# Optimization experiments

Hardware: AMD Instinct MI355X
Metric: run time of the kernel (lower is better)

## Reference

```python
import jax, jax.numpy as jnp
import numpy as np

D, H, W = 96, 320, 320          # sparse voxel grid spatial shape
N = 150000                      # number of active voxels
C_IN, C_OUT = 64, 64
EPS = 1e-5
NEG_SLOPE = 0.01


def setup_inputs() -> dict:
    key = jax.random.key(0)
    k1, k2 = jax.random.split(key)
    # unique active voxel coordinates (no collisions), like a real sparse tensor
    rng = np.random.default_rng(0)
    lin = rng.choice(D * H * W, size=N, replace=False)
    z, rem = lin // (H * W), lin % (H * W)
    y, x = rem // W, rem % W
    coords = jnp.asarray(np.stack([z, y, x], axis=1), dtype=jnp.int32)  # [N,3]
    features = jax.random.normal(k1, (N, C_IN), dtype=jnp.float32)
    # conv weight: one [Cin,Cout] matrix per 3x3x3 kernel offset
    weight = jax.random.normal(k2, (27, C_IN, C_OUT), dtype=jnp.float32) * (1.0 / np.sqrt(27 * C_IN))
    gamma = jnp.ones((C_OUT,), dtype=jnp.float32)
    beta = jnp.zeros((C_OUT,), dtype=jnp.float32)
    return {"features": features, "coords": coords, "weight": weight, "gamma": gamma, "beta": beta}


def reference(features, coords, weight, gamma, beta):
    # Submanifold sparse 3D conv: output sites == input sites (active voxels).
    # Build dense index grid: voxel coord -> row index in `features`, -1 if inactive.
    grid = jnp.full((D, H, W), -1, dtype=jnp.int32)
    grid = grid.at[coords[:, 0], coords[:, 1], coords[:, 2]].set(
        jnp.arange(features.shape[0], dtype=jnp.int32))

    out = jnp.zeros((features.shape[0], weight.shape[2]), dtype=features.dtype)
    k = 0
    for dz in (-1, 0, 1):
        for dy in (-1, 0, 1):
            for dx in (-1, 0, 1):
                nz = coords[:, 0] + dz
                ny = coords[:, 1] + dy
                nx = coords[:, 2] + dx
                inb = ((nz >= 0) & (nz < D) & (ny >= 0) & (ny < H)
                       & (nx >= 0) & (nx < W))
                idx = grid[jnp.clip(nz, 0, D - 1),
                           jnp.clip(ny, 0, H - 1),
                           jnp.clip(nx, 0, W - 1)]          # [N]
                valid = inb & (idx >= 0)
                gathered = jnp.where(valid[:, None],
                                     features[jnp.maximum(idx, 0)], 0.0)  # [N,Cin]
                out = out + gathered @ weight[k]             # gather-GEMM-scatter
                k += 1

    # BatchNorm1d (training-mode batch stats, biased variance) + LeakyReLU(0.01)
    mean = jnp.mean(out, axis=0)
    var = jnp.mean(jnp.square(out - mean), axis=0)
    xhat = (out - mean) * jax.lax.rsqrt(var + EPS)
    y = xhat * gamma + beta
    return jnp.where(y >= 0, y, NEG_SLOPE * y)
```

## Files before the change

kernel.cpp:

```cpp
#include <hip/hip_runtime.h>


#define DD 96
#define HH 320
#define WW 320
#define GRID_ELEMS (DD * HH * WW)
#define OCC_WORDS (GRID_ELEMS / 32)
#define CIN 64
#define COUT 64
#define PAIR_CAP 16384
#define STAGE_CAP 40
#define TILE_R 128
#define FSTRIDE 68
#define EPSV 1e-5f
#define SLOPE 0.01f

__global__ void scatter_k(const int* __restrict__ coords, int* __restrict__ grid,
                          unsigned* __restrict__ occ, int N) {
    int i = blockIdx.x * 256 + threadIdx.x;
    if (i >= N) return;
    int z = coords[3 * i], y = coords[3 * i + 1], x = coords[3 * i + 2];
    int l = (z * HH + y) * WW + x;
    grid[l] = i;
    atomicOr(&occ[l >> 5], 1u << (l & 31));
}

__global__ void rulebook_k(const int* __restrict__ coords, const int* __restrict__ grid,
                           const unsigned* __restrict__ occ,
                           int* __restrict__ cnt, int2* __restrict__ pairs, int N) {
    __shared__ int scnt[27];
    __shared__ int sbase[27];
    __shared__ int2 stage[27][STAGE_CAP];
    int tid = threadIdx.x;
    if (tid < 27) scnt[tid] = 0;
    __syncthreads();

    int i = blockIdx.x * 256 + tid;
    if (i < N) {
        int z = coords[3 * i], y = coords[3 * i + 1], x = coords[3 * i + 2];
        int lo = x > 0 ? x - 1 : 0;
        int hi = x < WW - 1 ? x + 1 : WW - 1;
        int wlo = lo >> 5, whi = hi >> 5;

        unsigned wa[9], wb9[9];
        int rwb[9];
#pragma unroll
        for (int r = 0; r < 9; ++r) {
            int zz = z + r / 3 - 1;
            int yy = y + r % 3 - 1;
            bool ok = ((unsigned)zz < DD) && ((unsigned)yy < HH);
            int base = (zz * HH + yy) * WW;
            rwb[r] = base;
            int wbase = base >> 5;
            wa[r]  = ok ? occ[wbase + wlo] : 0u;
            wb9[r] = ok ? occ[wbase + whi] : 0u;
        }
#pragma unroll
        for (int r = 0; r < 9; ++r) {
            for (int xx = lo; xx <= hi; ++xx) {
                if (r == 4 && xx == x) continue;
                unsigned w = ((xx >> 5) == wlo) ? wa[r] : wb9[r];
                if ((w >> (xx & 31)) & 1u) {
                    int j = grid[rwb[r] + xx];
                    int k = r * 3 + (xx - x + 1);
                    int pos = atomicAdd(&scnt[k], 1);
                    if (pos < STAGE_CAP) stage[k][pos] = make_int2(i, j);
                }
            }
        }
    }
    __syncthreads();
    if (tid < 27) {
        int c = scnt[tid];
        if (c > STAGE_CAP) c = STAGE_CAP;
        scnt[tid] = c;
        if (c > 0) sbase[tid] = atomicAdd(&cnt[tid * 32], c);
    }
    __syncthreads();
    for (int s = tid; s < 27 * STAGE_CAP; s += 256) {
        int k = s / STAGE_CAP, p = s % STAGE_CAP;
        if (p < scnt[k]) {
            int pos = sbase[k] + p;
            if (pos < PAIR_CAP) pairs[k * PAIR_CAP + pos] = stage[k][p];
        }
    }
}

__global__ void __launch_bounds__(256) center_k(const float* __restrict__ feat,
                                                const float* __restrict__ w13,
                                                float* __restrict__ out, int N) {
    __shared__ float wl[CIN * COUT];
    __shared__ float fl[TILE_R * FSTRIDE];
    {
        const float4* ws4 = (const float4*)w13;
        float4* wl4 = (float4*)wl;
        for (int t = threadIdx.x; t < CIN * COUT / 4; t += 256) wl4[t] = ws4[t];
    }
    int base_row = blockIdx.x * TILE_R;
    for (int t = threadIdx.x; t < TILE_R * 16; t += 256) {
        int r = t >> 4, c4 = t & 15;
        int gr = base_row + r;
        float4 v = (gr < N) ? ((const float4*)feat)[(size_t)gr * 16 + c4]
                            : make_float4(0.f, 0.f, 0.f, 0.f);
        *(float4*)&fl[r * FSTRIDE + c4 * 4] = v;
    }
    __syncthreads();

    int g = threadIdx.x >> 3;
    int c0 = (threadIdx.x & 7) * 8;
    float4 acc[4][2];
#pragma unroll
    for (int r = 0; r < 4; ++r) {
        acc[r][0] = make_float4(0.f, 0.f, 0.f, 0.f);
        acc[r][1] = make_float4(0.f, 0.f, 0.f, 0.f);
    }
#pragma unroll 4
    for (int ci4 = 0; ci4 < 16; ++ci4) {
        float4 f[4];
#pragma unroll
        for (int r = 0; r < 4; ++r)
            f[r] = *(const float4*)&fl[(g + 32 * r) * FSTRIDE + ci4 * 4];
#pragma unroll
        for (int u = 0; u < 4; ++u) {
            float4 wa = *(const float4*)&wl[(ci4 * 4 + u) * COUT + c0];
            float4 wb = *(const float4*)&wl[(ci4 * 4 + u) * COUT + c0 + 4];
#pragma unroll
            for (int r = 0; r < 4; ++r) {
                float fv = (&f[r].x)[u];
                acc[r][0].x += fv * wa.x;
                acc[r][0].y += fv * wa.y;
                acc[r][0].z += fv * wa.z;
                acc[r][0].w += fv * wa.w;
                acc[r][1].x += fv * wb.x;
                acc[r][1].y += fv * wb.y;
                acc[r][1].z += fv * wb.z;
                acc[r][1].w += fv * wb.w;
            }
        }
    }
    float4* o4 = (float4*)out;
#pragma unroll
    for (int r = 0; r < 4; ++r) {
        int row = base_row + g + 32 * r;
        if (row < N) {
            size_t base = (size_t)row * 16 + (c0 >> 2);
            o4[base] = acc[r][0];
            o4[base + 1] = acc[r][1];
        }
    }
}

__global__ void __launch_bounds__(256) offset_k(const float* __restrict__ feat,
                                                const float* __restrict__ weight,
                                                const int2* __restrict__ pairs,
                                                const int* __restrict__ cnt,
                                                float* __restrict__ out) {
    int k = blockIdx.y;
    if (k >= 13) ++k;
    int ck = cnt[k * 32];
    if (ck > PAIR_CAP) ck = PAIR_CAP;
    if ((int)blockIdx.x * 8 >= ck) return;
    __shared__ float wl[CIN * COUT];
    {
        const float4* ws4 = (const float4*)(weight + (size_t)k * CIN * COUT);
        float4* wl4 = (float4*)wl;
        for (int t = threadIdx.x; t < CIN * COUT / 4; t += 256) wl4[t] = ws4[t];
    }
    __syncthreads();
    int wave = threadIdx.x >> 6;
    int lane = threadIdx.x & 63;
    for (int p0 = (int)blockIdx.x * 8 + wave * 2; p0 < ck; p0 += (int)gridDim.x * 8) {
        bool hasB = (p0 + 1) < ck;
        int2 prA = pairs[k * PAIR_CAP + p0];
        int2 prB = pairs[k * PAIR_CAP + (hasB ? p0 + 1 : p0)];
        const float4* frA = (const float4*)(feat + (size_t)prA.y * CIN);
        const float4* frB = (const float4*)(feat + (size_t)prB.y * CIN);
        float accA = 0.f, accB = 0.f;
#pragma unroll
        for (int ci4 = 0; ci4 < 16; ++ci4) {
            float4 fa = frA[ci4];
            float4 fb = frB[ci4];
#pragma unroll
            for (int u = 0; u < 4; ++u) {
                float w = wl[(ci4 * 4 + u) * COUT + lane];
                accA += (&fa.x)[u] * w;
                accB += (&fb.x)[u] * w;
            }
        }
        atomicAdd(&out[(size_t)prA.x * COUT + lane], accA);
        if (hasB) atomicAdd(&out[(size_t)prB.x * COUT + lane], accB);
    }
}

__global__ void stats_k(const float* __restrict__ out, float* __restrict__ stats, int N) {
    __shared__ float ssum[4][64];
    __shared__ float ssq[4][64];
    int c = threadIdx.x & 63, g = threadIdx.x >> 6;
    float s = 0.f, q = 0.f;
    for (int r = blockIdx.x * 4 + g; r < N; r += gridDim.x * 4) {
        float v = out[(size_t)r * 64 + c];
        s += v;
        q += v * v;
    }
    ssum[g][c] = s;
    ssq[g][c] = q;
    __syncthreads();
    if (threadIdx.x < 64) {
        float ts = ssum[0][c] + ssum[1][c] + ssum[2][c] + ssum[3][c];
        float tq = ssq[0][c] + ssq[1][c] + ssq[2][c] + ssq[3][c];
        atomicAdd(&stats[c * 32], ts);
        atomicAdd(&stats[(64 + c) * 32], tq);
    }
}

__global__ void norm_k(float* __restrict__ out, const float* __restrict__ stats,
                       const float* __restrict__ gamma, const float* __restrict__ beta, int N) {
    int idx = (int)blockIdx.x * 256 + threadIdx.x;
    int total = N * (COUT / 4);
    if (idx >= total) return;
    int c0 = (idx & 15) * 4;
    float inv = 1.0f / (float)N;
    float4 v = ((const float4*)out)[idx];
    float4 r;
#pragma unroll
    for (int u = 0; u < 4; ++u) {
        int c = c0 + u;
        float mean = stats[c * 32] * inv;
        float var = stats[(64 + c) * 32] * inv - mean * mean;
        if (var < 0.f) var = 0.f;
        float sc = gamma[c] * rsqrtf(var + EPSV);
        float sh = beta[c] - mean * sc;
        float y = (&v.x)[u] * sc + sh;
        (&r.x)[u] = (y >= 0.f) ? y : SLOPE * y;
    }
    ((float4*)out)[idx] = r;
}

extern "C" void kernel_launch(void* const* d_in, const int* in_sizes, int n_in,
                              void* d_out, int out_size, void* d_ws, size_t ws_size,
                              hipStream_t stream) {
    const float* feat   = (const float*)d_in[0];
    const int*   coords = (const int*)d_in[1];
    const float* weight = (const float*)d_in[2];
    const float* gamma  = (const float*)d_in[3];
    const float* beta   = (const float*)d_in[4];
    float* out = (float*)d_out;
    int N = in_sizes[0] / CIN;

    char* ws = (char*)d_ws;
    int* grid = (int*)ws;
    size_t off = (size_t)GRID_ELEMS * 4;
    int* cnt = (int*)(ws + off);
    float* stats = (float*)(ws + off + 4096);
    int2* pairs = (int2*)(ws + off + 4096 + 16384);
    size_t occ_off = off + 4096 + 16384 + (size_t)27 * PAIR_CAP * 8;
    unsigned* occ = (unsigned*)(ws + occ_off);

    hipMemsetAsync(ws + off, 0, 4096 + 16384, stream);
    hipMemsetAsync(occ, 0, (size_t)OCC_WORDS * 4, stream);

    int nb = (N + 255) / 256;
    scatter_k<<<nb, 256, 0, stream>>>(coords, grid, occ, N);
    rulebook_k<<<nb, 256, 0, stream>>>(coords, grid, occ, cnt, pairs, N);
    int nbc = (N + TILE_R - 1) / TILE_R;
    center_k<<<nbc, 256, 0, stream>>>(feat, weight + 13 * CIN * COUT, out, N);
    offset_k<<<dim3(64, 26), 256, 0, stream>>>(feat, weight, pairs, cnt, out);
    stats_k<<<256, 256, 0, stream>>>(out, stats, N);
    int nb4 = (N * (COUT / 4) + 255) / 256;
    norm_k<<<nb4, 256, 0, stream>>>(out, stats, gamma, beta, N);
}
```

Measured before the change: 275.9 us.

## Transpose weights in LDS, vectorize stats, merge memsets, widen grids

The offset kernel now stores each weight matrix transposed and XOR-swizzled in shared memory, so each lane reads a float4 of weights per four input channels instead of four scalar loads. The stats kernel reads float4 rows with 16 row-groups per block and runs with more blocks. The two workspace memsets become one by placing the occupancy bitmap right after the stats area, and the offset kernel grid is widened. Together these target LDS load count, memory-access width and launch overhead, at the cost of more global atomics in stats and a strided transposing weight load.

```diff
diff --git a/kernel.cpp b/kernel.cpp
--- a/kernel.cpp
+++ b/kernel.cpp
@@ -160,15 +160,27 @@
     int ck = cnt[k * 32];
     if (ck > PAIR_CAP) ck = PAIR_CAP;
     if ((int)blockIdx.x * 8 >= ck) return;
-    __shared__ float wl[CIN * COUT];
+    __shared__ float wlT[CIN * COUT];
     {
-        const float4* ws4 = (const float4*)(weight + (size_t)k * CIN * COUT);
-        float4* wl4 = (float4*)wl;
-        for (int t = threadIdx.x; t < CIN * COUT / 4; t += 256) wl4[t] = ws4[t];
+        int c = threadIdx.x & 63;
+        int q4 = threadIdx.x >> 6;
+        const float* wk = weight + (size_t)k * CIN * COUT;
+        int sw = c & 7;
+#pragma unroll
+        for (int r = 0; r < 4; ++r) {
+            int ci4 = q4 * 4 + r;
+            float4 v;
+            v.x = wk[(ci4 * 4 + 0) * COUT + c];
+            v.y = wk[(ci4 * 4 + 1) * COUT + c];
+            v.z = wk[(ci4 * 4 + 2) * COUT + c];
+            v.w = wk[(ci4 * 4 + 3) * COUT + c];
+            *(float4*)&wlT[(c << 6) + ((ci4 ^ sw) << 2)] = v;
+        }
     }
     __syncthreads();
     int wave = threadIdx.x >> 6;
     int lane = threadIdx.x & 63;
+    int sw = lane & 7;
     for (int p0 = (int)blockIdx.x * 8 + wave * 2; p0 < ck; p0 += (int)gridDim.x * 8) {
         bool hasB = (p0 + 1) < ck;
         int2 prA = pairs[k * PAIR_CAP + p0];
@@ -178,14 +190,11 @@
         float accA = 0.f, accB = 0.f;
 #pragma unroll
         for (int ci4 = 0; ci4 < 16; ++ci4) {
+            float4 w = *(const float4*)&wlT[(lane << 6) + ((ci4 ^ sw) << 2)];
             float4 fa = frA[ci4];
             float4 fb = frB[ci4];
-#pragma unroll
-            for (int u = 0; u < 4; ++u) {
-                float w = wl[(ci4 * 4 + u) * COUT + lane];
-                accA += (&fa.x)[u] * w;
-                accB += (&fb.x)[u] * w;
-            }
+            accA += fa.x * w.x + fa.y * w.y + fa.z * w.z + fa.w * w.w;
+            accB += fb.x * w.x + fb.y * w.y + fb.z * w.z + fb.w * w.w;
         }
         atomicAdd(&out[(size_t)prA.x * COUT + lane], accA);
         if (hasB) atomicAdd(&out[(size_t)prB.x * COUT + lane], accB);
@@ -193,23 +202,33 @@
 }
 
 __global__ void stats_k(const float* __restrict__ out, float* __restrict__ stats, int N) {
-    __shared__ float ssum[4][64];
-    __shared__ float ssq[4][64];
-    int c = threadIdx.x & 63, g = threadIdx.x >> 6;
-    float s = 0.f, q = 0.f;
-    for (int r = blockIdx.x * 4 + g; r < N; r += gridDim.x * 4) {
-        float v = out[(size_t)r * 64 + c];
-        s += v;
-        q += v * v;
-    }
-    ssum[g][c] = s;
-    ssq[g][c] = q;
+    __shared__ float ssum[16][64];
+    __shared__ float ssq[16][64];
+    int c4 = threadIdx.x & 15;
+    int g = threadIdx.x >> 4;
+    float s0 = 0.f, s1 = 0.f, s2 = 0.f, s3 = 0.f;
+    float q0 = 0.f, q1 = 0.f, q2 = 0.f, q3 = 0.f;
+    for (int r = blockIdx.x * 16 + g; r < N; r += gridDim.x * 16) {
+        float4 v = ((const float4*)out)[(size_t)r * 16 + c4];
+        s0 += v.x; q0 += v.x * v.x;
+        s1 += v.y; q1 += v.y * v.y;
+        s2 += v.z; q2 += v.z * v.z;
+        s3 += v.w; q3 += v.w * v.w;
+    }
+    ssum[g][c4 * 4 + 0] = s0; ssq[g][c4 * 4 + 0] = q0;
+    ssum[g][c4 * 4 + 1] = s1; ssq[g][c4 * 4 + 1] = q1;
+    ssum[g][c4 * 4 + 2] = s2; ssq[g][c4 * 4 + 2] = q2;
+    ssum[g][c4 * 4 + 3] = s3; ssq[g][c4 * 4 + 3] = q3;
     __syncthreads();
     if (threadIdx.x < 64) {
-        float ts = ssum[0][c] + ssum[1][c] + ssum[2][c] + ssum[3][c];
-        float tq = ssq[0][c] + ssq[1][c] + ssq[2][c] + ssq[3][c];
-        atomicAdd(&stats[c * 32], ts);
-        atomicAdd(&stats[(64 + c) * 32], tq);
+        float ts = 0.f, tq = 0.f;
+#pragma unroll
+        for (int gg = 0; gg < 16; ++gg) {
+            ts += ssum[gg][threadIdx.x];
+            tq += ssq[gg][threadIdx.x];
+        }
+        atomicAdd(&stats[threadIdx.x * 32], ts);
+        atomicAdd(&stats[(64 + threadIdx.x) * 32], tq);
     }
 }
 
@@ -252,20 +271,18 @@
     size_t off = (size_t)GRID_ELEMS * 4;
     int* cnt = (int*)(ws + off);
     float* stats = (float*)(ws + off + 4096);
-    int2* pairs = (int2*)(ws + off + 4096 + 16384);
-    size_t occ_off = off + 4096 + 16384 + (size_t)27 * PAIR_CAP * 8;
-    unsigned* occ = (unsigned*)(ws + occ_off);
-
-    hipMemsetAsync(ws + off, 0, 4096 + 16384, stream);
-    hipMemsetAsync(occ, 0, (size_t)OCC_WORDS * 4, stream);
+    unsigned* occ = (unsigned*)(ws + off + 4096 + 16384);
+    int2* pairs = (int2*)(ws + off + 4096 + 16384 + (size_t)OCC_WORDS * 4);
+
+    hipMemsetAsync(ws + off, 0, 4096 + 16384 + (size_t)OCC_WORDS * 4, stream);
 
     int nb = (N + 255) / 256;
     scatter_k<<<nb, 256, 0, stream>>>(coords, grid, occ, N);
     rulebook_k<<<nb, 256, 0, stream>>>(coords, grid, occ, cnt, pairs, N);
     int nbc = (N + TILE_R - 1) / TILE_R;
     center_k<<<nbc, 256, 0, stream>>>(feat, weight + 13 * CIN * COUT, out, N);
-    offset_k<<<dim3(64, 26), 256, 0, stream>>>(feat, weight, pairs, cnt, out);
-    stats_k<<<256, 256, 0, stream>>>(out, stats, N);
+    offset_k<<<dim3(96, 26), 256, 0, stream>>>(feat, weight, pairs, cnt, out);
+    stats_k<<<1024, 256, 0, stream>>>(out, stats, N);
     int nb4 = (N * (COUT / 4) + 255) / 256;
     norm_k<<<nb4, 256, 0, stream>>>(out, stats, gamma, beta, N);
 }
```

Measured after the change: 258.4 us. 1.07x faster.
